# Kernel optimization log

Measured on AMD Instinct MI355X. Metric: run time of the kernel, lower is better.

Reference implementation:

```python
import jax, jax.numpy as jnp
import numpy as np

B, L, D, K = 16, 2048, 128, 8192
NUM_RQ_STEPS = 1


def _nearest(residual, codebook):
    # residual: [B,L,D], codebook: [K,D]
    d2 = (
        jnp.sum(residual * residual, axis=-1, keepdims=True)  # [B,L,1]
        - 2.0 * jnp.einsum('bld,kd->blk', residual, codebook)  # [B,L,K]
        + jnp.sum(codebook * codebook, axis=-1)  # [K]
    )
    idx = jnp.argmin(d2, axis=-1)  # [B,L]
    return codebook[idx], idx  # gather: [B,L,D]


def setup_inputs() -> dict:
    key = jax.random.key(0)
    k1, k2 = jax.random.split(key)
    z_e = jax.random.normal(k1, (B, L, D), dtype=jnp.float32)
    codebook = jax.random.normal(k2, (K, D), dtype=jnp.float32)
    return {"z_e": z_e, "codebook": codebook}


def reference(z_e, codebook):
    # apply_codebook(z_e, code_sg=True): codebook is stop-gradiented,
    # residual quantization over NUM_RQ_STEPS, straight-through on output.
    cb = jax.lax.stop_gradient(codebook)
    residual = z_e
    z_q = jnp.zeros_like(z_e)
    idx_list = []
    for _ in range(NUM_RQ_STEPS):
        q, idx = _nearest(residual, cb)
        z_q = z_q + q
        residual = residual - q
        idx_list.append(idx)
    indices = jnp.stack(idx_list, axis=-1)  # [B,L,num_rq_steps]
    # straight-through estimator (code_sg=True): grads flow to z_e, not codebook
    z_q = z_e + jax.lax.stop_gradient(z_q - z_e)
    return z_q, indices
```

## Files before the change

kernel.cpp:

```cpp
#include <hip/hip_runtime.h>


#define M_TOK  32768
#define DIM    128
#define KCODES 8192
#define BM     64
#define NT     (KCODES / 256)
#define MARGIN 0.10f
#define RTG    8

typedef _Float16 half8v __attribute__((ext_vector_type(8)));
typedef float float4v __attribute__((ext_vector_type(4)));

union H2U { _Float16 h; unsigned short u; };
__device__ __forceinline__ unsigned short f2h_bits(_Float16 h) {
  H2U c; c.h = h; return c.u;
}

__device__ __forceinline__ void gload_lds16(const void* g, void* l) {
  __builtin_amdgcn_global_load_lds(
      (const __attribute__((address_space(1))) unsigned int*)g,
      (__attribute__((address_space(3))) unsigned int*)l, 16, 0, 0);
}

#define CNORM_OFF  (KCODES * 256)
#define QCNT_OFF   (CNORM_OFF + KCODES * 4)
#define QTOK_OFF   (QCNT_OFF + 64)
#define KMIN_OFF   (QTOK_OFF + M_TOK * 4)

__global__ __launch_bounds__(256) void prep_kernel(
    const float* __restrict__ cb, unsigned short* __restrict__ Cs,
    float* __restrict__ cnorm, int* __restrict__ qcnt) {
  if (blockIdx.x == 0 && threadIdx.x == 0) *qcnt = 0;
  const int k = blockIdx.x * 4 + (threadIdx.x >> 6);
  const int lane = threadIdx.x & 63;
  const float2 v = ((const float2*)(cb + (size_t)k * DIM))[lane];
  float s = v.x * v.x + v.y * v.y;
  #pragma unroll
  for (int off = 32; off > 0; off >>= 1) s += __shfl_down(s, off);
  if (lane == 0) cnorm[k] = s;
  ushort2 hi;
  hi.x = f2h_bits((_Float16)v.x);
  hi.y = f2h_bits((_Float16)v.y);
  *(ushort2*)(Cs + (size_t)k * 128 + lane * 2) = hi;
}

__global__ __launch_bounds__(256, 2) void vq_mfma_kernel(
    const float* __restrict__ ze, const unsigned short* __restrict__ Cs,
    const float* __restrict__ cnorm, const float* __restrict__ cb,
    int* __restrict__ qcnt, int* __restrict__ qtok,
    unsigned long long* __restrict__ kmin,
    float* __restrict__ out_zq, float* __restrict__ out_idx) {
  __shared__ char lds[49152];
  char* const As = lds;
  char* const Bs = lds + 16384;

  const int tid = threadIdx.x;
  const int wn = tid >> 6;
  const int lane = tid & 63;
  const int quad = lane >> 4;
  const int l15 = lane & 15;
  const int m0 = blockIdx.x * BM;

  int loffC[4];
  #pragma unroll
  for (int c = 0; c < 4; ++c) {
    const int r = c * 16 + (lane >> 2);
    const int s = lane & 3;
    const int seg = s ^ ((r >> 1) & 3);
    loffC[c] = (wn * 64 + r) * 256 + seg * 16;
  }
  int boff[4];
  #pragma unroll
  for (int j = 0; j < 4; ++j) {
    const int n = j * 16 + l15;
    boff[j] = n * 64 + ((quad ^ ((n >> 1) & 3)) << 4);
  }
  char* const BsW = Bs + wn * 8192;

  {
    const int r = tid >> 2;
    const int qh = tid & 3;
    const float* zrow = ze + (size_t)(m0 + r) * DIM + qh * 32;
    char* arow = As + r * 256;
    const int rx = r & 7;
    #pragma unroll
    for (int i = 0; i < 8; ++i) {
      const float4 v = *(const float4*)(zrow + i * 4);
      ushort4 hh;
      hh.x = f2h_bits((_Float16)v.x);
      hh.y = f2h_bits((_Float16)v.y);
      hh.z = f2h_bits((_Float16)v.z);
      hh.w = f2h_bits((_Float16)v.w);
      const int c = qh * 32 + i * 4;
      *(ushort4*)(arow + ((((c >> 3) ^ rx) << 4) | ((c & 7) << 1))) = hh;
    }
  }
  __syncthreads();

  half8v ahi[4][4];
  #pragma unroll
  for (int ks = 0; ks < 4; ++ks)
    #pragma unroll
    for (int i = 0; i < 4; ++i) {
      const int m = i * 16 + l15;
      const int kslot = ks * 4 + quad;
      ahi[ks][i] = *(const half8v*)(As + m * 256 + ((kslot ^ (m & 7)) << 4));
    }

  float bestv[16], secv[16], idxv[16];
  #pragma unroll
  for (int s = 0; s < 16; ++s) {
    bestv[s] = 3.4e38f; secv[s] = 3.4e38f; idxv[s] = 0.f;
  }

  for (int nt = 0; nt < NT; ++nt) {
    const char* const tile = (const char*)Cs + (size_t)nt * 65536;
    float cnv[4];
    #pragma unroll
    for (int j = 0; j < 4; ++j)
      cnv[j] = cnorm[nt * 256 + wn * 64 + j * 16 + l15];

    float4v acc[4][4];
    #pragma unroll
    for (int i = 0; i < 4; ++i)
      #pragma unroll
      for (int j = 0; j < 4; ++j) acc[i][j] = (float4v)0.0f;

    #pragma unroll
    for (int t = 0; t < 2; ++t) {
      __syncthreads();
      #pragma unroll
      for (int p = 0; p < 2; ++p)
        #pragma unroll
        for (int c = 0; c < 4; ++c)
          gload_lds16(tile + (t * 2 + p) * 64 + loffC[c],
                      BsW + p * 4096 + c * 1024);
      __syncthreads();

      #pragma unroll
      for (int p = 0; p < 2; ++p) {
        const int kk = t * 2 + p;
        half8v bf[4];
        #pragma unroll
        for (int j = 0; j < 4; ++j)
          bf[j] = *(const half8v*)(BsW + p * 4096 + boff[j]);
        #pragma unroll
        for (int i = 0; i < 4; ++i)
          #pragma unroll
          for (int j = 0; j < 4; ++j)
            acc[i][j] = __builtin_amdgcn_mfma_f32_16x16x32_f16(
                ahi[kk][i], bf[j], acc[i][j], 0, 0, 0);
      }
    }

    #pragma unroll
    for (int j = 0; j < 4; ++j) {
      const float nidx = (float)(nt * 256 + wn * 64 + j * 16 + l15);
      const float cn = cnv[j];
      #pragma unroll
      for (int i = 0; i < 4; ++i)
        #pragma unroll
        for (int rg = 0; rg < 4; ++rg) {
          const float sc = fmaf(-2.0f, acc[i][j][rg], cn);
          const int slot = i * 4 + rg;
          const bool bt = sc < bestv[slot];
          secv[slot] = bt ? bestv[slot] : fminf(secv[slot], sc);
          idxv[slot] = bt ? nidx : idxv[slot];
          bestv[slot] = bt ? sc : bestv[slot];
        }
    }
  }

  #pragma unroll
  for (int slot = 0; slot < 16; ++slot) {
    float b = bestv[slot], sec = secv[slot], ix = idxv[slot];
    #pragma unroll
    for (int mk = 1; mk <= 8; mk <<= 1) {
      const float ob = __shfl_xor(b, mk);
      const float os = __shfl_xor(sec, mk);
      const float oi = __shfl_xor(ix, mk);
      const bool take = (ob < b) || (ob == b && oi < ix);
      const float loser = take ? b : ob;
      b = take ? ob : b;
      ix = take ? oi : ix;
      sec = fminf(fminf(sec, os), loser);
    }
    bestv[slot] = b; secv[slot] = sec; idxv[slot] = ix;
  }

  __syncthreads();
  float* const redB = (float*)lds;
  float* const redS = redB + 256;
  float* const redI = redB + 512;
  float* const lidxs = redB + 768;
  if (l15 == 0) {
    #pragma unroll
    for (int slot = 0; slot < 16; ++slot) {
      const int row = (slot >> 2) * 16 + quad * 4 + (slot & 3);
      redB[wn * 64 + row] = bestv[slot];
      redS[wn * 64 + row] = secv[slot];
      redI[wn * 64 + row] = idxv[slot];
    }
  }
  __syncthreads();
  if (tid < 64) {
    float b = redB[tid], sec = redS[tid], ix = redI[tid];
    #pragma unroll
    for (int w = 1; w < 4; ++w) {
      const float ob = redB[w * 64 + tid];
      const float os = redS[w * 64 + tid];
      const float oi = redI[w * 64 + tid];
      const bool take = (ob < b) || (ob == b && oi < ix);
      const float loser = take ? b : ob;
      b = take ? ob : b;
      ix = take ? oi : ix;
      sec = fminf(fminf(sec, os), loser);
    }
    out_idx[m0 + tid] = ix;
    lidxs[tid] = ix;
    if (sec - b < MARGIN) {
      kmin[m0 + tid] = ~0ull;
      const int p = atomicAdd(qcnt, 1);
      qtok[p] = m0 + tid;
    }
  }
  __syncthreads();

  const int tl = tid >> 2, qp = tid & 3;
  const int code = (int)lidxs[tl];
  const float4* src = (const float4*)(cb + (size_t)code * DIM);
  float4* dst = (float4*)(out_zq + (size_t)(m0 + tl) * DIM);
  #pragma unroll
  for (int p = 0; p < 8; ++p) dst[qp + p * 4] = src[qp + p * 4];
}

__global__ __launch_bounds__(256) void rescan_part_kernel(
    const float* __restrict__ ze, const float* __restrict__ cb,
    const float* __restrict__ cnorm, const int* __restrict__ qcnt,
    const int* __restrict__ qtok, unsigned long long* __restrict__ kmin) {
  __shared__ float xsh[RTG][132];
  __shared__ unsigned long long wpart[4][RTG];
  const int tid = threadIdx.x;
  const int wv = tid >> 6;
  const int lane = tid & 63;
  const int cg = blockIdx.x & 7;
  const int n = *qcnt;
  const int nslots = gridDim.x >> 3;
  const int c0 = cg * 1024 + tid;

  for (int g = blockIdx.x >> 3; g * RTG < n; g += nslots) {
    const int cnt = min(RTG, n - g * RTG);
    __syncthreads();
    if ((tid >> 5) < cnt) {
      const int token = qtok[g * RTG + (tid >> 5)];
      const float4 v =
          ((const float4*)(ze + (size_t)token * DIM))[tid & 31];
      ((float4*)(xsh[tid >> 5]))[tid & 31] = v;
    }
    __syncthreads();

    float dot[4][RTG];
    #pragma unroll
    for (int k = 0; k < 4; ++k)
      #pragma unroll
      for (int t = 0; t < RTG; ++t) dot[k][t] = 0.f;

    const float* crow0 = cb + (size_t)c0 * DIM;
    for (int d = 0; d < DIM; d += 4) {
      float4 x4[RTG];
      #pragma unroll
      for (int t = 0; t < RTG; ++t)
        x4[t] = *(const float4*)(xsh[t] + d);
      #pragma unroll
      for (int k = 0; k < 4; ++k) {
        const float4 c4 = *(const float4*)(crow0 + (size_t)k * 256 * DIM + d);
        #pragma unroll
        for (int t = 0; t < RTG; ++t) {
          dot[k][t] = fmaf(c4.x, x4[t].x, dot[k][t]);
          dot[k][t] = fmaf(c4.y, x4[t].y, dot[k][t]);
          dot[k][t] = fmaf(c4.z, x4[t].z, dot[k][t]);
          dot[k][t] = fmaf(c4.w, x4[t].w, dot[k][t]);
        }
      }
    }

    float cn[4];
    #pragma unroll
    for (int k = 0; k < 4; ++k) cn[k] = cnorm[c0 + k * 256];

    #pragma unroll
    for (int t = 0; t < RTG; ++t) {
      float s = fmaf(-2.f, dot[0][t], cn[0]);
      int ix = c0;
      #pragma unroll
      for (int k = 1; k < 4; ++k) {
        const float sk = fmaf(-2.f, dot[k][t], cn[k]);
        if (sk < s) { s = sk; ix = c0 + k * 256; }
      }
      #pragma unroll
      for (int mk = 1; mk <= 32; mk <<= 1) {
        const float os = __shfl_xor(s, mk);
        const int oi = __shfl_xor(ix, mk);
        if (os < s || (os == s && oi < ix)) { s = os; ix = oi; }
      }
      if (lane == 0) {
        union { float f; unsigned u; } c; c.f = s;
        const unsigned m = (c.u >> 31) ? ~c.u : (c.u | 0x80000000u);
        wpart[wv][t] = ((unsigned long long)m << 32) | (unsigned)ix;
      }
    }
    __syncthreads();
    if (tid < cnt) {
      unsigned long long k = wpart[0][tid];
      #pragma unroll
      for (int w = 1; w < 4; ++w) k = min(k, wpart[w][tid]);
      atomicMin(&kmin[qtok[g * RTG + tid]], k);
    }
  }
}

__global__ __launch_bounds__(256) void rescan_apply_kernel(
    const float* __restrict__ cb, const int* __restrict__ qcnt,
    const int* __restrict__ qtok, const unsigned long long* __restrict__ kmin,
    float* __restrict__ out_zq, float* __restrict__ out_idx) {
  const int tid = threadIdx.x;
  const int n = *qcnt;
  for (int qi = blockIdx.x; qi < n; qi += gridDim.x) {
    const int token = qtok[qi];
    const int code = (int)(unsigned int)(kmin[token] & 0xFFFFFFFFull);
    if (tid == 0) out_idx[token] = (float)code;
    if (tid < 32)
      ((float4*)(out_zq + (size_t)token * DIM))[tid] =
          ((const float4*)(cb + (size_t)code * DIM))[tid];
  }
}

extern "C" void kernel_launch(void* const* d_in, const int* in_sizes, int n_in,
                              void* d_out, int out_size, void* d_ws,
                              size_t ws_size, hipStream_t stream) {
  const float* ze = (const float*)d_in[0];
  const float* cb = (const float*)d_in[1];
  float* out = (float*)d_out;

  unsigned short* Cs = (unsigned short*)d_ws;
  float* cnorm = (float*)((char*)d_ws + CNORM_OFF);
  int* qcnt = (int*)((char*)d_ws + QCNT_OFF);
  int* qtok = (int*)((char*)d_ws + QTOK_OFF);
  unsigned long long* kmin = (unsigned long long*)((char*)d_ws + KMIN_OFF);

  prep_kernel<<<KCODES / 4, 256, 0, stream>>>(cb, Cs, cnorm, qcnt);
  vq_mfma_kernel<<<M_TOK / BM, 256, 0, stream>>>(
      ze, Cs, cnorm, cb, qcnt, qtok, kmin, out, out + (size_t)M_TOK * DIM);
  rescan_part_kernel<<<4096, 256, 0, stream>>>(ze, cb, cnorm, qcnt, qtok,
                                               kmin);
  rescan_apply_kernel<<<256, 256, 0, stream>>>(cb, qcnt, qtok, kmin, out,
                                               out + (size_t)M_TOK * DIM);
}
```

Before: 255.9 us.

## Split codebook search across two blocks per token tile and merge partials

Each 64-token tile is now handled by two blocks, each scanning half of the codebook (split-K over codes). This doubles the grid from 512 to 1024 blocks, which should fill the CUs more evenly. Partial best/second/index values go to workspace, and a new merge_gather kernel combines them, flags near-ties for rescan, and gathers the codebook rows. The cost is an extra kernel launch, extra partial-result traffic, and the A tile being loaded and converted twice. LDS per block shrinks from 48 KB to 32 KB.

```diff
diff --git a/kernel.cpp b/kernel.cpp
--- a/kernel.cpp
+++ b/kernel.cpp
@@ -5,7 +5,7 @@
 #define DIM    128
 #define KCODES 8192
 #define BM     64
-#define NT     (KCODES / 256)
+#define NT     16
 #define MARGIN 0.10f
 #define RTG    8
 
@@ -27,6 +27,9 @@
 #define QCNT_OFF   (CNORM_OFF + KCODES * 4)
 #define QTOK_OFF   (QCNT_OFF + 64)
 #define KMIN_OFF   (QTOK_OFF + M_TOK * 4)
+#define PARTB_OFF  (KMIN_OFF + M_TOK * 8)
+#define PARTS_OFF  (PARTB_OFF + M_TOK * 8)
+#define PARTI_OFF  (PARTS_OFF + M_TOK * 8)
 
 __global__ __launch_bounds__(256) void prep_kernel(
     const float* __restrict__ cb, unsigned short* __restrict__ Cs,
@@ -47,20 +50,20 @@
 
 __global__ __launch_bounds__(256, 2) void vq_mfma_kernel(
     const float* __restrict__ ze, const unsigned short* __restrict__ Cs,
-    const float* __restrict__ cnorm, const float* __restrict__ cb,
-    int* __restrict__ qcnt, int* __restrict__ qtok,
-    unsigned long long* __restrict__ kmin,
-    float* __restrict__ out_zq, float* __restrict__ out_idx) {
-  __shared__ char lds[49152];
+    const float* __restrict__ cnorm,
+    float* __restrict__ partB, float* __restrict__ partS,
+    float* __restrict__ partI) {
+  __shared__ char lds[32768];
   char* const As = lds;
-  char* const Bs = lds + 16384;
 
   const int tid = threadIdx.x;
   const int wn = tid >> 6;
   const int lane = tid & 63;
   const int quad = lane >> 4;
   const int l15 = lane & 15;
-  const int m0 = blockIdx.x * BM;
+  const int m0 = (blockIdx.x >> 1) * BM;
+  const int kh = blockIdx.x & 1;
+  const int cbase = kh * 4096;
 
   int loffC[4];
   #pragma unroll
@@ -76,7 +79,7 @@
     const int n = j * 16 + l15;
     boff[j] = n * 64 + ((quad ^ ((n >> 1) & 3)) << 4);
   }
-  char* const BsW = Bs + wn * 8192;
+  char* const BsW = lds + wn * 8192;
 
   {
     const int r = tid >> 2;
@@ -115,11 +118,12 @@
   }
 
   for (int nt = 0; nt < NT; ++nt) {
-    const char* const tile = (const char*)Cs + (size_t)nt * 65536;
+    const char* const tile =
+        (const char*)Cs + (size_t)cbase * 256 + (size_t)nt * 65536;
     float cnv[4];
     #pragma unroll
     for (int j = 0; j < 4; ++j)
-      cnv[j] = cnorm[nt * 256 + wn * 64 + j * 16 + l15];
+      cnv[j] = cnorm[cbase + nt * 256 + wn * 64 + j * 16 + l15];
 
     float4v acc[4][4];
     #pragma unroll
@@ -156,7 +160,7 @@
 
     #pragma unroll
     for (int j = 0; j < 4; ++j) {
-      const float nidx = (float)(nt * 256 + wn * 64 + j * 16 + l15);
+      const float nidx = (float)(cbase + nt * 256 + wn * 64 + j * 16 + l15);
       const float cn = cnv[j];
       #pragma unroll
       for (int i = 0; i < 4; ++i)
@@ -193,7 +197,6 @@
   float* const redB = (float*)lds;
   float* const redS = redB + 256;
   float* const redI = redB + 512;
-  float* const lidxs = redB + 768;
   if (l15 == 0) {
     #pragma unroll
     for (int slot = 0; slot < 16; ++slot) {
@@ -217,22 +220,47 @@
       ix = take ? oi : ix;
       sec = fminf(fminf(sec, os), loser);
     }
-    out_idx[m0 + tid] = ix;
-    lidxs[tid] = ix;
+    const int token = m0 + tid;
+    partB[token * 2 + kh] = b;
+    partS[token * 2 + kh] = sec;
+    partI[token * 2 + kh] = ix;
+  }
+}
+
+__global__ __launch_bounds__(256) void merge_gather_kernel(
+    const float* __restrict__ cb,
+    const float* __restrict__ partB, const float* __restrict__ partS,
+    const float* __restrict__ partI,
+    int* __restrict__ qcnt, int* __restrict__ qtok,
+    unsigned long long* __restrict__ kmin,
+    float* __restrict__ out_zq, float* __restrict__ out_idx) {
+  __shared__ float lidx[32];
+  const int tid = threadIdx.x;
+  const int t0 = blockIdx.x * 32;
+  if (tid < 32) {
+    const int token = t0 + tid;
+    const float b0 = partB[token * 2 + 0], b1 = partB[token * 2 + 1];
+    const float s0 = partS[token * 2 + 0], s1 = partS[token * 2 + 1];
+    const float i0 = partI[token * 2 + 0], i1 = partI[token * 2 + 1];
+    const bool take = b1 < b0;
+    const float b = take ? b1 : b0;
+    const float ix = take ? i1 : i0;
+    const float sec = fminf(fmaxf(b0, b1), fminf(s0, s1));
+    out_idx[token] = ix;
+    lidx[tid] = ix;
     if (sec - b < MARGIN) {
-      kmin[m0 + tid] = ~0ull;
+      kmin[token] = ~0ull;
       const int p = atomicAdd(qcnt, 1);
-      qtok[p] = m0 + tid;
+      qtok[p] = token;
     }
   }
   __syncthreads();
-
-  const int tl = tid >> 2, qp = tid & 3;
-  const int code = (int)lidxs[tl];
+  const int tl = tid >> 3, qp = tid & 7;
+  const int code = (int)lidx[tl];
   const float4* src = (const float4*)(cb + (size_t)code * DIM);
-  float4* dst = (float4*)(out_zq + (size_t)(m0 + tl) * DIM);
-  #pragma unroll
-  for (int p = 0; p < 8; ++p) dst[qp + p * 4] = src[qp + p * 4];
+  float4* dst = (float4*)(out_zq + (size_t)(t0 + tl) * DIM);
+  #pragma unroll
+  for (int p = 0; p < 4; ++p) dst[qp + p * 8] = src[qp + p * 8];
 }
 
 __global__ __launch_bounds__(256) void rescan_part_kernel(
@@ -348,10 +376,16 @@
   int* qcnt = (int*)((char*)d_ws + QCNT_OFF);
   int* qtok = (int*)((char*)d_ws + QTOK_OFF);
   unsigned long long* kmin = (unsigned long long*)((char*)d_ws + KMIN_OFF);
+  float* partB = (float*)((char*)d_ws + PARTB_OFF);
+  float* partS = (float*)((char*)d_ws + PARTS_OFF);
+  float* partI = (float*)((char*)d_ws + PARTI_OFF);
 
   prep_kernel<<<KCODES / 4, 256, 0, stream>>>(cb, Cs, cnorm, qcnt);
-  vq_mfma_kernel<<<M_TOK / BM, 256, 0, stream>>>(
-      ze, Cs, cnorm, cb, qcnt, qtok, kmin, out, out + (size_t)M_TOK * DIM);
+  vq_mfma_kernel<<<(M_TOK / BM) * 2, 256, 0, stream>>>(
+      ze, Cs, cnorm, partB, partS, partI);
+  merge_gather_kernel<<<M_TOK / 32, 256, 0, stream>>>(
+      cb, partB, partS, partI, qcnt, qtok, kmin, out,
+      out + (size_t)M_TOK * DIM);
   rescan_part_kernel<<<4096, 256, 0, stream>>>(ze, cb, cnorm, qcnt, qtok,
                                                kmin);
   rescan_apply_kernel<<<256, 256, 0, stream>>>(cb, qcnt, qtok, kmin, out,
```

After: 274.3 us. 1.07x slower.
